# Kernel optimization log

Hardware: AMD Instinct MI355X
Metric: run time of the kernel (lower is better)

## Reference

```python
import jax, jax.numpy as jnp
import numpy as np

N_HEADS = 4
N_NODES = 10000
EMB = 128
N_BATCH = 4096
N_NEAREST = 8
N_SENTINELS = 8


def setup_inputs() -> dict:
    key = jax.random.key(0)
    k1, k2, k3, k4 = jax.random.split(key, 4)
    embeds = jax.random.normal(k1, (N_HEADS, N_NODES, EMB), jnp.float32)
    field = jax.random.uniform(k3, (N_HEADS, N_NODES, EMB), dtype=jnp.float32)
    uncertainty = jnp.ones((1, 1, 1), jnp.float32) * 5.0
    adj = (jax.random.uniform(k4, (N_NODES, N_NODES)) < 0.001).astype(jnp.float32)
    batch_edges = jax.random.randint(k2, (2, N_BATCH), 0, N_NODES)
    return {"embeds": embeds, "field": field, "uncertainty": uncertainty,
            "adj": adj, "batch_edges": batch_edges}


def _knn_samples(embeds, nodes, k):
    # embeds: (h, n, d); nodes: (b,) -> indices of k nearest neighbors, excluding self.
    # Squared L2 distance is monotone in L2 norm, so top-k order matches the
    # original's .norm(dim=3).topk(..., largest=False).
    x = embeds[:, nodes]                                  # (h, b, d)
    x2 = jnp.sum(x * x, axis=-1)[:, :, None]              # (h, b, 1)
    y2 = jnp.sum(embeds * embeds, axis=-1)[:, None, :]    # (h, 1, n)
    d2 = x2 + y2 - 2.0 * jnp.einsum('hbd,hnd->hbn', x, embeds)  # (h, b, n)
    _, idx = jax.lax.top_k(-d2, k + 1)                    # nearest first
    return jax.lax.stop_gradient(idx[:, :, 1:])           # drop self -> (h, b, k)


def reference(embeds, field, uncertainty, adj, batch_edges):
    src, dst = batch_edges[0], batch_edges[1]
    h_idx = jnp.arange(N_HEADS)[:, None, None]

    def build(nodes, nodes_logits, adj_gather):
        samples = _knn_samples(embeds, nodes, N_NEAREST)                 # (h,b,k)
        diff = embeds[:, nodes][:, :, None, :] - embeds[h_idx, samples]  # (h,b,k,d)
        label = uncertainty * (adj_gather(samples) * 2.0 - 1.0)          # (h,b,k)
        g = field[:, nodes_logits]                                        # (h,b,d)
        logits = jnp.einsum('hbkd,hbd->hbk', diff, g) + label
        return logits, diff

    src_logits, src_diff = build(src, dst, lambda s: adj[s, dst[None, :, None]])
    tgt_logits, tgt_diff = build(dst, src, lambda s: adj[src[None, :, None], s])

    logits = jnp.concatenate([src_logits, tgt_logits], axis=2)           # (h,b,2k)
    dist = jnp.linalg.norm(jnp.concatenate([src_diff, tgt_diff], axis=2), axis=3)

    h, b = logits.shape[0], logits.shape[1]
    logits = jnp.concatenate(
        [logits, jnp.zeros((h, b, N_SENTINELS), logits.dtype)], axis=2)
    dist = jnp.concatenate(
        [dist, jnp.ones((h, b, N_SENTINELS), dist.dtype)], axis=2)

    # softmin: softmax(1 - dist)-weighted sum of logits, then mean over heads
    softmin = jnp.sum(logits * jax.nn.softmax(1.0 - dist, axis=2), axis=2)  # (h,b)
    return jax.nn.sigmoid(softmin.mean(axis=0)).reshape(-1)                 # (b,)
```

## Files before the change

### kernel.cpp

```cpp
#include <hip/hip_runtime.h>
#include <math.h>
#include <stdint.h>

#define N_HEADS 4
#define N_NODES 10000
#define NPAD 10112
#define NPG (NPAD / 32)
#define EMB 128
#define N_BATCH 4096
#define NQ (2 * N_BATCH)
#define K 8
#define TQ 32
#define TN 128
#define NTILES (NPAD / TN)
#define PH 2
#define CAP 41
#define WIN 0.5f

typedef __attribute__((ext_vector_type(8))) __bf16 bf16x8;
typedef __attribute__((ext_vector_type(8))) unsigned short ushortx8;
typedef __attribute__((ext_vector_type(16))) float floatx16;

__device__ __forceinline__ unsigned short f2bf(float x) {
  unsigned u = __float_as_uint(x);
  u += 0x7fff + ((u >> 16) & 1);
  return (unsigned short)(u >> 16);
}

__device__ __forceinline__ void insert8(float* bs, int* bi, float s, int node) {
  if (s < bs[K - 1]) {
    #pragma unroll
    for (int k2 = K - 1; k2 >= 0; --k2) {
      if (!(s < bs[k2])) break;
      if (k2 < K - 1) { bs[k2 + 1] = bs[k2]; bi[k2 + 1] = bi[k2]; }
      bs[k2] = s; bi[k2] = node;
    }
  }
}

__device__ __forceinline__ size_t pchunk(int g, int c, int lm) {
  return (size_t)g * 4096 + (size_t)(c >> 1) * 512 + (size_t)(c & 1) * 256 + lm * 8;
}

__global__ __launch_bounds__(256) void prep_kernel(
    const float* __restrict__ E, unsigned short* __restrict__ EhiP,
    float* __restrict__ y2g) {
  __shared__ float s_p[8][33];
  const int h = blockIdx.y, g = blockIdx.x;
  const int lm = threadIdx.x & 31, c8 = threadIdx.x >> 5;
  const int n = g * 32 + lm;
  float x[16];
  #pragma unroll
  for (int j = 0; j < 16; ++j) x[j] = 0.f;
  if (n < N_NODES) {
    const float* src = E + (size_t)(h * N_NODES + n) * EMB + c8 * 16;
    #pragma unroll
    for (int j = 0; j < 4; ++j) {
      float4 v = *(const float4*)(src + j * 4);
      x[j * 4 + 0] = v.x; x[j * 4 + 1] = v.y; x[j * 4 + 2] = v.z; x[j * 4 + 3] = v.w;
    }
  }
  float part = 0.f;
  ushortx8 hi[2];
  #pragma unroll
  for (int j = 0; j < 16; ++j) {
    part += x[j] * x[j];
    hi[j >> 3][j & 7] = f2bf(x[j]);
  }
  size_t base = (size_t)h * NPG * 4096;
  #pragma unroll
  for (int lh = 0; lh < 2; ++lh)
    *(ushortx8*)&EhiP[base + pchunk(g, c8 * 2 + lh, lm)] = hi[lh];
  s_p[c8][lm] = part;
  __syncthreads();
  if (threadIdx.x < 32) {
    int nn = g * 32 + threadIdx.x;
    float s = 0.f;
    #pragma unroll
    for (int j = 0; j < 8; ++j) s += s_p[j][threadIdx.x];
    y2g[h * NPAD + nn] = (nn < N_NODES) ? s : 1e30f;
  }
}

__global__ __launch_bounds__(256, 4) void knn_kernel(
    const unsigned short* __restrict__ EhiP, const float* __restrict__ y2g,
    const float* __restrict__ Ef, const int* __restrict__ be,
    int* __restrict__ samples) {
  __shared__ __align__(16) float s_x[TQ * TN];
  __shared__ float s_t8S[TQ * 9];
  __shared__ int   s_t8I[TQ * 9];
  __shared__ float s_lsS[TQ * CAP];
  __shared__ int   s_lsI[TQ * CAP];
  __shared__ float s_thr[TQ];
  __shared__ int   s_cnt[TQ];

  const int id = blockIdx.x;
  const int h = (id & 7) >> 1;
  const int qt = ((id >> 3) << 1) | (id & 1);
  const int tid = threadIdx.x;
  const int lane = tid & 63;
  const int w1 = tid >> 6;
  const int lm = lane & 31, lh = lane >> 5;
  const unsigned short* EhiH = EhiP + (size_t)h * NPG * 4096;
  const float* y2H = y2g + h * NPAD;
  const float* EH = Ef + (size_t)h * N_NODES * EMB;

  bf16x8 ahi[8];
  unsigned short* s_xq = (unsigned short*)s_x;
  {
    int r = tid >> 3, cb = (tid & 7) * 2;
    int rx15 = r & 15;
    int q = be[qt * TQ + r];
    int gq = q >> 5, lmq = q & 31;
    #pragma unroll
    for (int c = 0; c < 2; ++c) {
      int lc = cb + c;
      *(bf16x8*)&s_xq[r * EMB + (lc ^ rx15) * 8] =
          *(const bf16x8*)&EhiH[pchunk(gq, lc, lmq)];
    }
    __syncthreads();
    const int arx = lm & 15;
    #pragma unroll
    for (int ks = 0; ks < 8; ++ks)
      ahi[ks] = *(const bf16x8*)&s_xq[lm * EMB + (((ks * 2 + lh) ^ arx)) * 8];
    __syncthreads();
  }

  const int qsel = tid >> 3;
  const int csel = tid & 7;
  const int myq = be[qt * TQ + qsel];
  float bs[K]; int bi[K];
  #pragma unroll
  for (int k2 = 0; k2 < K; ++k2) { bs[k2] = 1e30f; bi[k2] = 0x7fffffff; }
  if (tid < TQ) s_cnt[tid] = 0;

  const int bnode = 32 * w1 + lm;
  const unsigned short* bhp = EhiH + (size_t)w1 * 4096 + lane * 8;

  #pragma unroll 1
  for (int t = 0; t < PH; ++t) {
    const size_t goff = (size_t)t * 16384;
    float ny = y2H[t * TN + bnode];
    floatx16 acc = {0.f, 0.f, 0.f, 0.f, 0.f, 0.f, 0.f, 0.f,
                    0.f, 0.f, 0.f, 0.f, 0.f, 0.f, 0.f, 0.f};
    #pragma unroll
    for (int ks = 0; ks < 8; ++ks) {
      bf16x8 vbh = *(const bf16x8*)(bhp + goff + ks * 512);
      acc = __builtin_amdgcn_mfma_f32_32x32x16_bf16(ahi[ks], vbh, acc, 0, 0, 0);
    }
    #pragma unroll
    for (int r = 0; r < 16; ++r) {
      int row = (r & 3) + 8 * (r >> 2) + 4 * lh;
      s_x[row * TN + bnode] = fmaf(-2.f, acc[r], ny);
    }
    __syncthreads();
    int nbp = t * TN;
    #pragma unroll
    for (int s = 0; s < 16; ++s) {
      int j = csel * 16 + ((s + qsel) & 15);
      float sc = s_x[qsel * TN + j];
      int node = nbp + j;
      if (node != myq) insert8(bs, bi, sc, node);
    }
    __syncthreads();
  }

  {
    float* scrS = (float*)s_x;
    int*   scrI = (int*)s_x + TQ * 64;
    #pragma unroll
    for (int k2 = 0; k2 < K; ++k2) {
      scrS[tid * 8 + k2] = bs[k2]; scrI[tid * 8 + k2] = bi[k2];
    }
    __syncthreads();
    if (tid < TQ) {
      int q = tid;
      float ts[K]; int ti[K];
      #pragma unroll
      for (int k2 = 0; k2 < K; ++k2) { ts[k2] = 1e30f; ti[k2] = 0x7fffffff; }
      for (int kk = 0; kk < 64; ++kk) {
        int e = (kk + q) & 63;
        insert8(ts, ti, scrS[q * 64 + e], scrI[q * 64 + e]);
      }
      float thr = ts[K - 1], win = thr + WIN;
      int nc = 0;
      for (int kk = 0; kk < 64; ++kk) {
        int e = (kk + q) & 63;
        float sv = scrS[q * 64 + e]; int iv = scrI[q * 64 + e];
        if (sv <= win && nc < CAP) {
          bool dup = false;
          #pragma unroll
          for (int j = 0; j < K; ++j) dup = dup || (ti[j] == iv);
          if (!dup) { s_lsS[q * CAP + nc] = sv; s_lsI[q * CAP + nc] = iv; ++nc; }
        }
      }
      s_cnt[q] = nc;
      s_thr[q] = win;
      #pragma unroll
      for (int k2 = 0; k2 < K; ++k2) { s_t8S[q * 9 + k2] = ts[k2]; s_t8I[q * 9 + k2] = ti[k2]; }
    }
    __syncthreads();
  }

  float thrf[16];
  #pragma unroll
  for (int r = 0; r < 16; ++r) thrf[r] = s_thr[(r & 3) + 8 * (r >> 2) + 4 * lh];

  #pragma unroll 1
  for (int t = PH; t < NTILES; ++t) {
    if (t == 4 || t == 8 || t == 16 || t == 32) {
      __syncthreads();
      if (tid < TQ) {
        int q = tid;
        int myqm = be[qt * TQ + q];
        float ts[K]; int ti[K];
        #pragma unroll
        for (int k2 = 0; k2 < K; ++k2) { ts[k2] = s_t8S[q * 9 + k2]; ti[k2] = s_t8I[q * 9 + k2]; }
        int cnt = s_cnt[q]; if (cnt > CAP) cnt = CAP;
        for (int p = 0; p < cnt; ++p) {
          int iv = s_lsI[q * CAP + p];
          if (iv != myqm) insert8(ts, ti, s_lsS[q * CAP + p], iv);
        }
        float thr = ts[K - 1], win = thr + WIN;
        int nc = 0;
        for (int p = 0; p < cnt; ++p) {
          float sv = s_lsS[q * CAP + p]; int iv = s_lsI[q * CAP + p];
          if (sv <= win && iv != myqm) {
            bool dup = false;
            #pragma unroll
            for (int j = 0; j < K; ++j) dup = dup || (ti[j] == iv);
            if (!dup && nc < CAP) { s_lsS[q * CAP + nc] = sv; s_lsI[q * CAP + nc] = iv; ++nc; }
          }
        }
        #pragma unroll
        for (int k2 = 0; k2 < K; ++k2) {
          float sv = s_t8S[q * 9 + k2]; int iv = s_t8I[q * 9 + k2];
          if (sv <= win && iv != myqm && nc < CAP) {
            bool dup = false;
            #pragma unroll
            for (int j = 0; j < K; ++j) dup = dup || (ti[j] == iv);
            if (!dup) { s_lsS[q * CAP + nc] = sv; s_lsI[q * CAP + nc] = iv; ++nc; }
          }
        }
        s_cnt[q] = nc;
        s_thr[q] = win;
        #pragma unroll
        for (int k2 = 0; k2 < K; ++k2) { s_t8S[q * 9 + k2] = ts[k2]; s_t8I[q * 9 + k2] = ti[k2]; }
      }
      __syncthreads();
      #pragma unroll
      for (int r = 0; r < 16; ++r) thrf[r] = s_thr[(r & 3) + 8 * (r >> 2) + 4 * lh];
    }

    const size_t goff = (size_t)t * 16384;
    float ny = y2H[t * TN + bnode];
    floatx16 acc = {0.f, 0.f, 0.f, 0.f, 0.f, 0.f, 0.f, 0.f,
                    0.f, 0.f, 0.f, 0.f, 0.f, 0.f, 0.f, 0.f};
    #pragma unroll
    for (int ks = 0; ks < 8; ++ks) {
      bf16x8 vbh = *(const bf16x8*)(bhp + goff + ks * 512);
      acc = __builtin_amdgcn_mfma_f32_32x32x16_bf16(ahi[ks], vbh, acc, 0, 0, 0);
    }
    const int node = t * TN + bnode;
    #pragma unroll
    for (int r = 0; r < 16; ++r) {
      float sc = fmaf(-2.f, acc[r], ny);
      if (sc < thrf[r]) {
        int q = (r & 3) + 8 * (r >> 2) + 4 * lh;
        int p = atomicAdd(&s_cnt[q], 1);
        if (p < CAP) { s_lsS[q * CAP + p] = sc; s_lsI[q * CAP + p] = node; }
      }
    }
  }

  __syncthreads();
  {
    int q = tid >> 3, k = tid & 7;
    int qn = be[qt * TQ + q];
    const float4* Eq = (const float4*)(EH + (size_t)qn * EMB);
    int iv = s_t8I[q * 9 + k];
    if (iv < N_NODES) {
      const float4* En = (const float4*)(EH + (size_t)iv * EMB);
      float d0 = 0.f, d1 = 0.f, d2 = 0.f, d3 = 0.f;
      #pragma unroll
      for (int d = 0; d < 32; ++d) {
        float4 a = Eq[d], b = En[d];
        d0 += a.x * b.x; d1 += a.y * b.y; d2 += a.z * b.z; d3 += a.w * b.w;
      }
      s_t8S[q * 9 + k] = y2H[iv] - 2.f * ((d0 + d1) + (d2 + d3));
    }
    int cnt = s_cnt[q]; if (cnt > CAP) cnt = CAP;
    for (int p = k; p < cnt; p += 8) {
      int jv = s_lsI[q * CAP + p];
      if (jv < N_NODES && jv != qn) {
        const float4* En = (const float4*)(EH + (size_t)jv * EMB);
        float d0 = 0.f, d1 = 0.f, d2 = 0.f, d3 = 0.f;
        #pragma unroll
        for (int d = 0; d < 32; ++d) {
          float4 a = Eq[d], b = En[d];
          d0 += a.x * b.x; d1 += a.y * b.y; d2 += a.z * b.z; d3 += a.w * b.w;
        }
        s_lsS[q * CAP + p] = y2H[jv] - 2.f * ((d0 + d1) + (d2 + d3));
      }
    }
  }
  __syncthreads();
  if (tid < TQ) {
    int q = tid;
    int myqm = be[qt * TQ + q];
    float ts[K]; int ti[K];
    #pragma unroll
    for (int k2 = 0; k2 < K; ++k2) { ts[k2] = 1e30f; ti[k2] = 0x7fffffff; }
    #pragma unroll
    for (int k2 = 0; k2 < K; ++k2)
      insert8(ts, ti, s_t8S[q * 9 + k2], s_t8I[q * 9 + k2]);
    int cnt = s_cnt[q]; if (cnt > CAP) cnt = CAP;
    for (int p = 0; p < cnt; ++p) {
      int iv = s_lsI[q * CAP + p];
      if (iv != myqm) insert8(ts, ti, s_lsS[q * CAP + p], iv);
    }
    size_t base = ((size_t)h * NQ + qt * TQ + q) * K;
    #pragma unroll
    for (int k2 = 0; k2 < K; ++k2) samples[base + k2] = ti[k2];
  }
}

__global__ __launch_bounds__(256) void predict_kernel(
    const float* __restrict__ E, const float* __restrict__ F,
    const float* __restrict__ unc, const float* __restrict__ adj,
    const int* __restrict__ be, const int* __restrict__ samples,
    float* __restrict__ out) {
  int b = blockIdx.x;
  int h = threadIdx.x >> 6;
  int lane = threadIdx.x & 63;
  __shared__ float smv[N_HEADS];

  int srcb = be[b];
  int dstb = be[N_BATCH + b];
  const float* Eh = E + (size_t)h * N_NODES * EMB;
  const float* Fh = F + (size_t)h * N_NODES * EMB;
  float2 es = *(const float2*)(Eh + (size_t)srcb * EMB + 2 * lane);
  float2 ed = *(const float2*)(Eh + (size_t)dstb * EMB + 2 * lane);
  float2 fs = *(const float2*)(Fh + (size_t)srcb * EMB + 2 * lane);
  float2 fd = *(const float2*)(Fh + (size_t)dstb * EMB + 2 * lane);
  float u = unc[0];

  float logit[16], dist[16];
  #pragma unroll
  for (int j = 0; j < 16; ++j) {
    bool isrc = (j < 8);
    int qrow = isrc ? b : (N_BATCH + b);
    int s = samples[((size_t)h * NQ + qrow) * K + (j & 7)];
    float2 ev = *(const float2*)(Eh + (size_t)s * EMB + 2 * lane);
    float2 bb = isrc ? es : ed;
    float2 g = isrc ? fd : fs;
    float dx = bb.x - ev.x, dy = bb.y - ev.y;
    float dot = dx * g.x + dy * g.y;
    float nrm = dx * dx + dy * dy;
    #pragma unroll
    for (int o = 32; o > 0; o >>= 1) {
      dot += __shfl_xor(dot, o);
      nrm += __shfl_xor(nrm, o);
    }
    float a = isrc ? adj[(size_t)s * N_NODES + dstb]
                   : adj[(size_t)srcb * N_NODES + s];
    logit[j] = dot + u * (2.0f * a - 1.0f);
    dist[j] = sqrtf(nrm);
  }

  float m = 0.0f;
  #pragma unroll
  for (int j = 0; j < 16; ++j) m = fmaxf(m, 1.0f - dist[j]);
  float Z = 8.0f * expf(-m);
  float num = 0.0f;
  #pragma unroll
  for (int j = 0; j < 16; ++j) {
    float e = expf(1.0f - dist[j] - m);
    Z += e;
    num += logit[j] * e;
  }
  if (lane == 0) smv[h] = num / Z;
  __syncthreads();
  if (threadIdx.x == 0) {
    float t = 0.25f * (smv[0] + smv[1] + smv[2] + smv[3]);
    out[b] = 1.0f / (1.0f + expf(-t));
  }
}

extern "C" void kernel_launch(void* const* d_in, const int* in_sizes, int n_in,
                              void* d_out, int out_size, void* d_ws,
                              size_t ws_size, hipStream_t stream) {
  const float* E = (const float*)d_in[0];
  const float* F = (const float*)d_in[1];
  const float* U = (const float*)d_in[2];
  const float* A = (const float*)d_in[3];
  const int* be = (const int*)d_in[4];
  float* out = (float*)d_out;

  char* w = (char*)d_ws;
  unsigned short* EhiP = (unsigned short*)(w);
  float* y2g = (float*)(w + 10354688);
  int* samples = (int*)(w + 10516736);

  prep_kernel<<<dim3(NPG, N_HEADS), 256, 0, stream>>>(E, EhiP, y2g);
  knn_kernel<<<dim3((NQ / TQ) * N_HEADS), 256, 0, stream>>>(EhiP, y2g, E, be, samples);
  predict_kernel<<<dim3(N_BATCH), 256, 0, stream>>>(E, F, U, A, be, samples, out);
}
```

Before: 777.2 us.

## Double-buffer B tile loads, move A fragments to LDS, pack thresholds as bf16

The scan loop is unrolled by two. The next tile's B fragments and norms are prefetched into registers while the current tile's MFMA runs. The query A fragments are no longer held in 8 vector registers; each MFMA step rereads them from a dedicated shared-memory buffer. The 16 per-row thresholds are packed as rounded-up bf16 pairs into 8 registers. Together these free registers for the double buffer, at the cost of extra LDS reads and slightly looser thresholds, which admit a few more candidates into the candidate lists.

Measured after the change: 1.114 ms. 1.43x slower.

```diff
diff --git a/kernel.cpp b/kernel.cpp
--- a/kernel.cpp
+++ b/kernel.cpp
@@ -26,6 +26,10 @@
   u += 0x7fff + ((u >> 16) & 1);
   return (unsigned short)(u >> 16);
 }
+__device__ __forceinline__ uint32_t bfup(float f) {
+  uint32_t u = __float_as_uint(f);
+  return (f >= 0.f) ? ((u + 0xFFFFu) >> 16) : (u >> 16);
+}
 
 __device__ __forceinline__ void insert8(float* bs, int* bi, float s, int node) {
   if (s < bs[K - 1]) {
@@ -87,6 +91,7 @@
     const float* __restrict__ Ef, const int* __restrict__ be,
     int* __restrict__ samples) {
   __shared__ __align__(16) float s_x[TQ * TN];
+  __shared__ __align__(16) unsigned short s_ahi[TQ * EMB];
   __shared__ float s_t8S[TQ * 9];
   __shared__ int   s_t8I[TQ * 9];
   __shared__ float s_lsS[TQ * CAP];
@@ -105,8 +110,6 @@
   const float* y2H = y2g + h * NPAD;
   const float* EH = Ef + (size_t)h * N_NODES * EMB;
 
-  bf16x8 ahi[8];
-  unsigned short* s_xq = (unsigned short*)s_x;
   {
     int r = tid >> 3, cb = (tid & 7) * 2;
     int rx15 = r & 15;
@@ -115,14 +118,9 @@
     #pragma unroll
     for (int c = 0; c < 2; ++c) {
       int lc = cb + c;
-      *(bf16x8*)&s_xq[r * EMB + (lc ^ rx15) * 8] =
+      *(bf16x8*)&s_ahi[r * EMB + (lc ^ rx15) * 8] =
           *(const bf16x8*)&EhiH[pchunk(gq, lc, lmq)];
     }
-    __syncthreads();
-    const int arx = lm & 15;
-    #pragma unroll
-    for (int ks = 0; ks < 8; ++ks)
-      ahi[ks] = *(const bf16x8*)&s_xq[lm * EMB + (((ks * 2 + lh) ^ arx)) * 8];
     __syncthreads();
   }
 
@@ -135,6 +133,7 @@
   if (tid < TQ) s_cnt[tid] = 0;
 
   const int bnode = 32 * w1 + lm;
+  const int arx = lm & 15;
   const unsigned short* bhp = EhiH + (size_t)w1 * 4096 + lane * 8;
 
   #pragma unroll 1
@@ -145,8 +144,9 @@
                     0.f, 0.f, 0.f, 0.f, 0.f, 0.f, 0.f, 0.f};
     #pragma unroll
     for (int ks = 0; ks < 8; ++ks) {
+      bf16x8 va = *(const bf16x8*)&s_ahi[lm * EMB + (((ks * 2 + lh) ^ arx)) * 8];
       bf16x8 vbh = *(const bf16x8*)(bhp + goff + ks * 512);
-      acc = __builtin_amdgcn_mfma_f32_32x32x16_bf16(ahi[ks], vbh, acc, 0, 0, 0);
+      acc = __builtin_amdgcn_mfma_f32_32x32x16_bf16(va, vbh, acc, 0, 0, 0);
     }
     #pragma unroll
     for (int r = 0; r < 16; ++r) {
@@ -202,12 +202,48 @@
     __syncthreads();
   }
 
-  float thrf[16];
-  #pragma unroll
-  for (int r = 0; r < 16; ++r) thrf[r] = s_thr[(r & 3) + 8 * (r >> 2) + 4 * lh];
-
+  uint32_t thrp[8];
+  #pragma unroll
+  for (int j = 0; j < 8; ++j) {
+    int r0 = 2 * j, r1 = 2 * j + 1;
+    float t0 = s_thr[(r0 & 3) + 8 * (r0 >> 2) + 4 * lh];
+    float t1 = s_thr[(r1 & 3) + 8 * (r1 >> 2) + 4 * lh];
+    thrp[j] = bfup(t0) | (bfup(t1) << 16);
+  }
+
+  auto compute_tile = [&](int t, const bf16x8* vb, float ny) {
+    floatx16 acc = {0.f, 0.f, 0.f, 0.f, 0.f, 0.f, 0.f, 0.f,
+                    0.f, 0.f, 0.f, 0.f, 0.f, 0.f, 0.f, 0.f};
+    #pragma unroll
+    for (int ks = 0; ks < 8; ++ks) {
+      bf16x8 va = *(const bf16x8*)&s_ahi[lm * EMB + (((ks * 2 + lh) ^ arx)) * 8];
+      acc = __builtin_amdgcn_mfma_f32_32x32x16_bf16(va, vb[ks], acc, 0, 0, 0);
+    }
+    const int node = t * TN + bnode;
+    #pragma unroll
+    for (int r = 0; r < 16; ++r) {
+      float sc = fmaf(-2.f, acc[r], ny);
+      float th = (r & 1) ? __uint_as_float(thrp[r >> 1] & 0xFFFF0000u)
+                         : __uint_as_float(thrp[r >> 1] << 16);
+      if (sc < th) {
+        int q = (r & 3) + 8 * (r >> 2) + 4 * lh;
+        int p = atomicAdd(&s_cnt[q], 1);
+        if (p < CAP) { s_lsS[q * CAP + p] = sc; s_lsI[q * CAP + p] = node; }
+      }
+    }
+  };
+
+  bf16x8 vb0[8], vb1[8];
+  float ny0 = 0.f, ny1 = 0.f;
+  {
+    const size_t goff = (size_t)PH * 16384;
+    ny0 = y2H[PH * TN + bnode];
+    #pragma unroll
+    for (int ks = 0; ks < 8; ++ks)
+      vb0[ks] = *(const bf16x8*)(bhp + goff + ks * 512);
+  }
   #pragma unroll 1
-  for (int t = PH; t < NTILES; ++t) {
+  for (int t = PH; t < NTILES; t += 2) {
     if (t == 4 || t == 8 || t == 16 || t == 32) {
       __syncthreads();
       if (tid < TQ) {
@@ -249,27 +285,31 @@
       }
       __syncthreads();
       #pragma unroll
-      for (int r = 0; r < 16; ++r) thrf[r] = s_thr[(r & 3) + 8 * (r >> 2) + 4 * lh];
-    }
-
-    const size_t goff = (size_t)t * 16384;
-    float ny = y2H[t * TN + bnode];
-    floatx16 acc = {0.f, 0.f, 0.f, 0.f, 0.f, 0.f, 0.f, 0.f,
-                    0.f, 0.f, 0.f, 0.f, 0.f, 0.f, 0.f, 0.f};
-    #pragma unroll
-    for (int ks = 0; ks < 8; ++ks) {
-      bf16x8 vbh = *(const bf16x8*)(bhp + goff + ks * 512);
-      acc = __builtin_amdgcn_mfma_f32_32x32x16_bf16(ahi[ks], vbh, acc, 0, 0, 0);
-    }
-    const int node = t * TN + bnode;
-    #pragma unroll
-    for (int r = 0; r < 16; ++r) {
-      float sc = fmaf(-2.f, acc[r], ny);
-      if (sc < thrf[r]) {
-        int q = (r & 3) + 8 * (r >> 2) + 4 * lh;
-        int p = atomicAdd(&s_cnt[q], 1);
-        if (p < CAP) { s_lsS[q * CAP + p] = sc; s_lsI[q * CAP + p] = node; }
-      }
+      for (int j = 0; j < 8; ++j) {
+        int r0 = 2 * j, r1 = 2 * j + 1;
+        float t0 = s_thr[(r0 & 3) + 8 * (r0 >> 2) + 4 * lh];
+        float t1 = s_thr[(r1 & 3) + 8 * (r1 >> 2) + 4 * lh];
+        thrp[j] = bfup(t0) | (bfup(t1) << 16);
+      }
+    }
+
+    if (t + 1 < NTILES) {
+      const size_t goff = (size_t)(t + 1) * 16384;
+      ny1 = y2H[(t + 1) * TN + bnode];
+      #pragma unroll
+      for (int ks = 0; ks < 8; ++ks)
+        vb1[ks] = *(const bf16x8*)(bhp + goff + ks * 512);
+    }
+    compute_tile(t, vb0, ny0);
+    if (t + 1 < NTILES) {
+      if (t + 2 < NTILES) {
+        const size_t goff = (size_t)(t + 2) * 16384;
+        ny0 = y2H[(t + 2) * TN + bnode];
+        #pragma unroll
+        for (int ks = 0; ks < 8; ++ks)
+          vb0[ks] = *(const bf16x8*)(bhp + goff + ks * 512);
+      }
+      compute_tile(t + 1, vb1, ny1);
     }
   }
 
```
